# Performance work log

Measured on AMD Instinct MI355X. Metric: run time of the kernel, lower is better.

Reference implementation:

```python
import jax, jax.numpy as jnp
import numpy as np
from jax import lax

SCALE = 2  # scale_factor

def _make_kernel():
    k1 = np.array([1.0, 3.0, 3.0, 1.0], dtype=np.float32)
    k2 = np.outer(k1, k1)
    k2 = k2 / k2.sum() * (SCALE ** 2)  # kernel_gain=None -> gain = scale_factor
    return jnp.asarray(k2)  # [4,4], symmetric so torch's flip(0,1) is a no-op


def setup_inputs() -> dict:
    key = jax.random.key(0)
    x = jax.random.normal(key, (16, 128, 128, 128), dtype=jnp.float32)  # NCHW
    return {"x": x, "kernel": _make_kernel()}


def reference(x, kernel):
    # dilated depthwise conv. torch pads a trailing zero after every pixel
    # (size 2H) then pads (top=2, bottom=1); lhs_dilation gives size 2H-1,
    # so symmetric padding (2,2) reproduces the exact same math.
    n, c, h, w = x.shape
    kh, kw = kernel.shape
    k4 = jnp.broadcast_to(kernel[None, None], (c, 1, kh, kw))  # depthwise OIHW
    out = lax.conv_general_dilated(
        x, k4,
        window_strides=(1, 1),
        padding=((2, 2), (2, 2)),
        lhs_dilation=(SCALE, SCALE),
        dimension_numbers=("NCHW", "OIHW", "NCHW"),
        feature_group_count=c,
    )  # [N, C, 2H, 2W]
    return out
```

## Files before the change

### kernel.cpp

```cpp
#include <hip/hip_runtime.h>


#define H  128
#define W  128
#define OH 256
#define OW 256

__global__ __launch_bounds__(256) void upsample2x_kernel(
    const float* __restrict__ x, float* __restrict__ out)
{
    const int tx = threadIdx.x;
    const int ty = threadIdx.y;
    const int iy = (blockIdx.x << 2) + ty;
    const int p  = blockIdx.y;

    const float* __restrict__ in = x + (size_t)p * (H * W);
    float*       __restrict__ o  = out + (size_t)p * (size_t)(OH * OW);

    const int K = tx << 1;

    const int   cl = (K == 0)     ? 0       : (K - 1);
    const float wl = (K == 0)     ? 0.0f    : 1.0f;
    const int   cr = (K == W - 2) ? (W - 1) : (K + 2);
    const float wr = (K == W - 2) ? 0.0f    : 1.0f;

    float h[3][4];
    #pragma unroll
    for (int r = 0; r < 3; ++r) {
        int ry  = iy - 1 + r;
        int ryc = ry < 0 ? 0 : (ry > H - 1 ? H - 1 : ry);
        const float* row = in + ryc * W;
        float2 m  = *(const float2*)(row + K);
        float a0  = row[cl] * wl;
        float a1  = m.x;
        float a2  = m.y;
        float a3  = row[cr] * wr;
        h[r][0] = 0.25f * a0 + 0.75f * a1;
        h[r][1] = 0.75f * a1 + 0.25f * a2;
        h[r][2] = 0.25f * a1 + 0.75f * a2;
        h[r][3] = 0.75f * a2 + 0.25f * a3;
    }

    const float w0 = (iy > 0)     ? 0.25f : 0.0f;
    const float w2 = (iy < H - 1) ? 0.25f : 0.0f;

    float4 ev, ov;
    ev.x = w0 * h[0][0] + 0.75f * h[1][0];
    ev.y = w0 * h[0][1] + 0.75f * h[1][1];
    ev.z = w0 * h[0][2] + 0.75f * h[1][2];
    ev.w = w0 * h[0][3] + 0.75f * h[1][3];
    ov.x = 0.75f * h[1][0] + w2 * h[2][0];
    ov.y = 0.75f * h[1][1] + w2 * h[2][1];
    ov.z = 0.75f * h[1][2] + w2 * h[2][2];
    ov.w = 0.75f * h[1][3] + w2 * h[2][3];

    float* orow = o + (size_t)(2 * iy) * OW + (tx << 2);
    *(float4*)(orow)      = ev;
    *(float4*)(orow + OW) = ov;
}

extern "C" void kernel_launch(void* const* d_in, const int* in_sizes, int n_in,
                              void* d_out, int out_size, void* d_ws, size_t ws_size,
                              hipStream_t stream)
{
    const float* x = (const float*)d_in[0];
    float* out = (float*)d_out;

    dim3 block(64, 4, 1);
    dim3 grid(H / 4, 16 * 128);
    upsample2x_kernel<<<grid, block, 0, stream>>>(x, out);
}
```

Baseline: 646.3 us.

## Stream rows per wavefront with register reuse and shuffle-based horizontal neighbors

Each wavefront now handles a 32-row strip of one plane. It walks down the rows, keeping the previous horizontally filtered row in registers, so each input row is read once instead of three times. Horizontal neighbors come from lane shuffles rather than extra scalar global loads. The grid shrinks to one block per plane, which cuts the number of blocks but gives each thread a serial loop and less parallelism to hide memory latency.

```diff
diff --git a/kernel.cpp b/kernel.cpp
--- a/kernel.cpp
+++ b/kernel.cpp
@@ -3,60 +3,99 @@
 
 #define H  128
 #define W  128
-#define OH 256
 #define OW 256
+#define CH 32
 
 __global__ __launch_bounds__(256) void upsample2x_kernel(
     const float* __restrict__ x, float* __restrict__ out)
 {
-    const int tx = threadIdx.x;
-    const int ty = threadIdx.y;
-    const int iy = (blockIdx.x << 2) + ty;
-    const int p  = blockIdx.y;
+    const int lane = threadIdx.x;
+    const int s    = (int)threadIdx.y * CH;
+    const int p    = blockIdx.x;
 
-    const float* __restrict__ in = x + (size_t)p * (H * W);
-    float*       __restrict__ o  = out + (size_t)p * (size_t)(OH * OW);
+    const float* __restrict__ in = x + (size_t)p * (H * W) + (lane << 1);
+    float*       __restrict__ o  = out + (size_t)p * (OW * OW) + (lane << 2);
 
-    const int K = tx << 1;
+    const float wl = (lane == 0)  ? 0.0f : 0.25f;
+    const float wr = (lane == 63) ? 0.0f : 0.25f;
 
-    const int   cl = (K == 0)     ? 0       : (K - 1);
-    const float wl = (K == 0)     ? 0.0f    : 1.0f;
-    const int   cr = (K == W - 2) ? (W - 1) : (K + 2);
-    const float wr = (K == W - 2) ? 0.0f    : 1.0f;
-
-    float h[3][4];
-    #pragma unroll
-    for (int r = 0; r < 3; ++r) {
-        int ry  = iy - 1 + r;
-        int ryc = ry < 0 ? 0 : (ry > H - 1 ? H - 1 : ry);
-        const float* row = in + ryc * W;
-        float2 m  = *(const float2*)(row + K);
-        float a0  = row[cl] * wl;
-        float a1  = m.x;
-        float a2  = m.y;
-        float a3  = row[cr] * wr;
-        h[r][0] = 0.25f * a0 + 0.75f * a1;
-        h[r][1] = 0.75f * a1 + 0.25f * a2;
-        h[r][2] = 0.25f * a1 + 0.75f * a2;
-        h[r][3] = 0.75f * a2 + 0.25f * a3;
+#define HROW(dst, m)                                         \
+    {                                                        \
+        float a0 = __shfl_up((m).y, 1);        \
+        float a3 = __shfl_down((m).x, 1);      \
+        (dst).x = wl * a0 + 0.75f * (m).x;                   \
+        (dst).y = 0.75f * (m).x + 0.25f * (m).y;             \
+        (dst).z = 0.25f * (m).x + 0.75f * (m).y;             \
+        (dst).w = 0.75f * (m).y + wr * a3;                   \
     }
 
-    const float w0 = (iy > 0)     ? 0.25f : 0.0f;
-    const float w2 = (iy < H - 1) ? 0.25f : 0.0f;
+    const float* rp   = in + s * W;
+    float*       orow = o + (size_t)(2 * s) * OW;
 
-    float4 ev, ov;
-    ev.x = w0 * h[0][0] + 0.75f * h[1][0];
-    ev.y = w0 * h[0][1] + 0.75f * h[1][1];
-    ev.z = w0 * h[0][2] + 0.75f * h[1][2];
-    ev.w = w0 * h[0][3] + 0.75f * h[1][3];
-    ov.x = 0.75f * h[1][0] + w2 * h[2][0];
-    ov.y = 0.75f * h[1][1] + w2 * h[2][1];
-    ov.z = 0.75f * h[1][2] + w2 * h[2][2];
-    ov.w = 0.75f * h[1][3] + w2 * h[2][3];
+    float4 hp;
+    if (s > 0) {
+        float2 m = *(const float2*)(rp - W);
+        HROW(hp, m);
+    } else {
+        hp = make_float4(0.0f, 0.0f, 0.0f, 0.0f);
+    }
 
-    float* orow = o + (size_t)(2 * iy) * OW + (tx << 2);
-    *(float4*)(orow)      = ev;
-    *(float4*)(orow + OW) = ov;
+    float2 mc = *(const float2*)rp;
+    float2 mn = *(const float2*)(rp + W);
+    rp += 2 * W;
+
+    {
+        float4 hc;
+        HROW(hc, mc);
+        float4 ve;
+        ve.x = 0.25f * hp.x + 0.75f * hc.x;
+        ve.y = 0.25f * hp.y + 0.75f * hc.y;
+        ve.z = 0.25f * hp.z + 0.75f * hc.z;
+        ve.w = 0.25f * hp.w + 0.75f * hc.w;
+        *(float4*)orow = ve;
+        hp = hc;
+        mc = mn;
+        orow += 2 * OW;
+    }
+
+    #pragma unroll 4
+    for (int i = s + 1; i < s + CH; ++i) {
+        float2 nx;
+        if (i < H - 1) nx = *(const float2*)rp;
+        else           nx = make_float2(0.0f, 0.0f);
+        rp += W;
+
+        float4 hc;
+        HROW(hc, mc);
+
+        float4 vo, ve;
+        vo.x = 0.75f * hp.x + 0.25f * hc.x;
+        vo.y = 0.75f * hp.y + 0.25f * hc.y;
+        vo.z = 0.75f * hp.z + 0.25f * hc.z;
+        vo.w = 0.75f * hp.w + 0.25f * hc.w;
+        ve.x = 0.25f * hp.x + 0.75f * hc.x;
+        ve.y = 0.25f * hp.y + 0.75f * hc.y;
+        ve.z = 0.25f * hp.z + 0.75f * hc.z;
+        ve.w = 0.25f * hp.w + 0.75f * hc.w;
+        *(float4*)(orow - OW) = vo;
+        *(float4*)(orow)      = ve;
+
+        hp = hc;
+        mc = nx;
+        orow += 2 * OW;
+    }
+
+    {
+        float4 hc;
+        HROW(hc, mc);
+        float4 vo;
+        vo.x = 0.75f * hp.x + 0.25f * hc.x;
+        vo.y = 0.75f * hp.y + 0.25f * hc.y;
+        vo.z = 0.75f * hp.z + 0.25f * hc.z;
+        vo.w = 0.75f * hp.w + 0.25f * hc.w;
+        *(float4*)(orow - OW) = vo;
+    }
+#undef HROW
 }
 
 extern "C" void kernel_launch(void* const* d_in, const int* in_sizes, int n_in,
@@ -67,6 +106,6 @@
     float* out = (float*)d_out;
 
     dim3 block(64, 4, 1);
-    dim3 grid(H / 4, 16 * 128);
+    dim3 grid(16 * 128, 1, 1);
     upsample2x_kernel<<<grid, block, 0, stream>>>(x, out);
 }
```

Measured after the change: 624.4 us. 3.4% less time.
